# Kernel tuning notes

Hardware: AMD Instinct MI355X
Metric: run time of the kernel (lower is better)

The kernel has to match this reference:

```python
import jax, jax.numpy as jnp
import numpy as np


def setup_inputs() -> dict:
    key = jax.random.key(0)
    k_x, k_B, k_C, k_D, k_step = jax.random.split(key, 5)
    Bsz, L, H = 8, 4096, 512
    P = 256  # effective state dim = dim_ssm_state // 2 (conj_sym)
    # s4d_inv init for Lambda (complex, stored as real/imag parts)
    n = jnp.arange(P, dtype=jnp.float32)
    Lambda_re = -0.5 * jnp.ones((P,), dtype=jnp.float32)
    Lambda_im = (P / np.pi) * (P / (2.0 * n + 1.0) - 1.0)
    # lecun_normal-ish init for B (P,H,2) and C (H,P,2), divided by sqrt(2)
    B = jax.random.normal(k_B, (P, H, 2), dtype=jnp.float32) * (1.0 / np.sqrt(H)) / np.sqrt(2.0)
    C = jax.random.normal(k_C, (H, P, 2), dtype=jnp.float32) * (1.0 / np.sqrt(P)) / np.sqrt(2.0)
    D = jax.random.normal(k_D, (H,), dtype=jnp.float32)
    dt_min, dt_max = 1e-3, 1e-1
    log_step = jax.random.uniform(k_step, (P,)) * (np.log(dt_max) - np.log(dt_min)) + np.log(dt_min)
    x = jax.random.normal(k_x, (Bsz, L, H), dtype=jnp.float32)
    return {"x": x, "Lambda_re": Lambda_re, "Lambda_im": Lambda_im,
            "B": B, "C": C, "D": D, "log_step": log_step.astype(jnp.float32)}


def _binary_op(q_i, q_j):
    A_i, b_i = q_i
    A_j, b_j = q_j
    return (A_j * A_i, A_j * b_i + b_j)


def reference(x, Lambda_re, Lambda_im, B, C, D, log_step):
    # Assemble complex params (conj_sym=True)
    Lam = Lambda_re + 1j * Lambda_im          # (P,)
    B_tilde = B[..., 0] + 1j * B[..., 1]      # (P,H)
    C_tilde = C[..., 0] + 1j * C[..., 1]      # (H,P)
    step = jnp.exp(log_step)                  # (P,) step_rescale = 1.0
    # ZOH discretization
    Lambda_bar = jnp.exp(Lam * step)                              # (P,)
    B_bar = ((Lambda_bar - 1.0) / Lam)[:, None] * B_tilde         # (P,H)
    # Bu elements: (Bsz, L, P) complex
    Bu = jnp.einsum('blh,ph->blp', x.astype(B_bar.dtype), B_bar)
    Lam_elems = jnp.broadcast_to(Lambda_bar, Bu.shape)
    # Parallel linear recurrence over time axis
    _, xs = jax.lax.associative_scan(_binary_op, (Lam_elems, Bu), axis=1)
    # Output projection with conjugate symmetry + D skip
    ys = 2.0 * jnp.einsum('blp,hp->blh', xs, C_tilde).real + D * x
    return ys
```

## Files before the change

kernel.cpp:

```cpp
#include <hip/hip_runtime.h>
#include <hip/hip_bf16.h>
#include <hip/hip_fp16.h>
#include <math.h>

#define BSZ 8
#define LSEQ 4096
#define HDIM 512
#define PDIM 256
#define MROWS (BSZ * LSEQ)
#define NDIM 512
#define CHUNK 32
#define NCHUNK (LSEQ / CHUNK)
#define LOG2CHUNK 5

typedef __attribute__((ext_vector_type(8))) short bf16x8;
typedef __attribute__((ext_vector_type(4))) float f32x4;

__global__ void precompute_params(const float* __restrict__ Lre,
                                  const float* __restrict__ Lim,
                                  const float* __restrict__ logstep,
                                  float* __restrict__ f_re, float* __restrict__ f_im,
                                  float* __restrict__ a_re, float* __restrict__ a_im,
                                  float* __restrict__ al_re, float* __restrict__ al_im) {
    int p = threadIdx.x;
    if (p >= PDIM) return;
    double step = exp((double)logstep[p]);
    double dlr = (double)Lre[p], dli = (double)Lim[p];
    double mag = exp(dlr * step);
    double ar = mag * cos(dli * step);
    double ai = mag * sin(dli * step);
    double den = dlr * dlr + dli * dli;
    double nr = ar - 1.0, ni = ai;
    f_re[p] = (float)((nr * dlr + ni * dli) / den);
    f_im[p] = (float)((ni * dlr - nr * dli) / den);
    a_re[p] = (float)ar;
    a_im[p] = (float)ai;
    double cr = ar, ci = ai;
#pragma unroll
    for (int i = 0; i < LOG2CHUNK; ++i) {
        double tr = cr * cr - ci * ci;
        double ti = 2.0 * cr * ci;
        cr = tr; ci = ti;
    }
    al_re[p] = (float)cr;
    al_im[p] = (float)ci;
}

#define NCONV (MROWS * HDIM / 4 / 256)
__global__ __launch_bounds__(256) void prep(
    const float* __restrict__ x, __hip_bfloat16* __restrict__ xb,
    const float* __restrict__ f_re, const float* __restrict__ f_im,
    const float* __restrict__ Bmat, __hip_bfloat16* __restrict__ W1T,
    const float* __restrict__ Cmat, __hip_bfloat16* __restrict__ W2T) {
    const int bid = blockIdx.x;
    const int tid = threadIdx.x;
    if (bid < NCONV) {
        int i = bid * 256 + tid;
        float4 v = ((const float4*)x)[i];
        union { ushort4 u; __hip_bfloat16 h[4]; } o;
        o.h[0] = __float2bfloat16(v.x);
        o.h[1] = __float2bfloat16(v.y);
        o.h[2] = __float2bfloat16(v.z);
        o.h[3] = __float2bfloat16(v.w);
        ((ushort4*)xb)[i] = o.u;
    } else if (bid < NCONV + 512) {
        int idx = (bid - NCONV) * 256 + tid;
        int p = idx / HDIM, h = idx % HDIM;
        float fr = f_re[p], fi = f_im[p];
        float br = Bmat[(size_t)(p * HDIM + h) * 2 + 0];
        float bi = Bmat[(size_t)(p * HDIM + h) * 2 + 1];
        W1T[(size_t)(2 * p) * HDIM + h]     = __float2bfloat16(fr * br - fi * bi);
        W1T[(size_t)(2 * p + 1) * HDIM + h] = __float2bfloat16(fr * bi + fi * br);
    } else {
        int idx = (bid - NCONV - 512) * 256 + tid;
        int h = idx / PDIM, p = idx % PDIM;
        float cr = Cmat[(size_t)(h * PDIM + p) * 2 + 0];
        float ci = Cmat[(size_t)(h * PDIM + p) * 2 + 1];
        W2T[(size_t)h * NDIM + 2 * p]     = __float2bfloat16(2.0f * cr);
        W2T[(size_t)h * NDIM + 2 * p + 1] = __float2bfloat16(-2.0f * ci);
    }
}

template <typename OT, bool SKIP>
__global__ __launch_bounds__(256) void gemm_bt(
    const __hip_bfloat16* __restrict__ A,
    const __hip_bfloat16* __restrict__ BT,
    OT* __restrict__ C,
    const float* __restrict__ Dvec,
    const __hip_bfloat16* __restrict__ Xskip,
    int M, int N, int K) {
    __shared__ __hip_bfloat16 smA[3 * 128 * 32];
    __shared__ __hip_bfloat16 smB[3 * 128 * 32];

    const int tid = threadIdx.x;
    const int lane = tid & 63;
    const int wave = tid >> 6;
    const int row0 = blockIdx.x * 128;
    const int col0 = blockIdx.y * 128;
    const int wm = (wave >> 1) * 64;
    const int wn = (wave & 1) * 64;

    const int sr = lane >> 2;
    const int swz_st = ((lane >> 2) & 3) ^ ((lane >> 4) & 3);
    const int sk = (((lane & 3) ^ swz_st) * 8);
    const int quad = lane >> 4;
    const int l15 = lane & 15;
    const int rq = ((quad ^ ((l15 & 3) ^ ((l15 >> 2) & 3))) * 8);

    f32x4 acc[4][4] = {};

    auto stage = [&](int buf, int t) {
        const int k0 = t << 5;
#pragma unroll
        for (int q = 0; q < 2; ++q) {
            const int chunk = wave * 32 + q * 16;
            const __hip_bfloat16* gA = A + (size_t)(row0 + chunk + sr) * K + k0 + sk;
            __builtin_amdgcn_global_load_lds(
                (const __attribute__((address_space(1))) void*)gA,
                (__attribute__((address_space(3))) void*)&smA[buf * 4096 + chunk * 32],
                16, 0, 0);
            const __hip_bfloat16* gB = BT + (size_t)(col0 + chunk + sr) * K + k0 + sk;
            __builtin_amdgcn_global_load_lds(
                (const __attribute__((address_space(1))) void*)gB,
                (__attribute__((address_space(3))) void*)&smB[buf * 4096 + chunk * 32],
                16, 0, 0);
        }
    };

    const int nk = K >> 5;
    stage(0, 0);
    stage(1, 1);
    asm volatile("s_waitcnt vmcnt(4)" ::: "memory");
    __builtin_amdgcn_s_barrier();

    int cur = 0;
    for (int t = 0; t < nk; ++t) {
        if (t + 2 < nk) {
            int st = cur + 2; if (st >= 3) st -= 3;
            stage(st, t + 2);
        }

        const __hip_bfloat16* sA = &smA[cur * 4096];
        const __hip_bfloat16* sB = &smB[cur * 4096];
        bf16x8 af[4], bfr[4];
#pragma unroll
        for (int i = 0; i < 4; ++i)
            af[i] = *(const bf16x8*)&sA[(wm + i * 16 + l15) * 32 + rq];
#pragma unroll
        for (int j = 0; j < 4; ++j)
            bfr[j] = *(const bf16x8*)&sB[(wn + j * 16 + l15) * 32 + rq];
#pragma unroll
        for (int i = 0; i < 4; ++i)
#pragma unroll
            for (int j = 0; j < 4; ++j)
                acc[i][j] = __builtin_amdgcn_mfma_f32_16x16x32_bf16(
                    af[i], bfr[j], acc[i][j], 0, 0, 0);

        if (t + 1 < nk) {
            if (t + 2 < nk)
                asm volatile("s_waitcnt vmcnt(4)" ::: "memory");
            else
                asm volatile("s_waitcnt vmcnt(0)" ::: "memory");
            __builtin_amdgcn_s_barrier();
        }
        cur += 1; if (cur == 3) cur = 0;
    }

#pragma unroll
    for (int i = 0; i < 4; ++i) {
        const int mbase = row0 + wm + i * 16 + quad * 4;
#pragma unroll
        for (int j = 0; j < 4; ++j) {
            const int col = col0 + wn + j * 16 + l15;
            const float dv = SKIP ? Dvec[col] : 0.0f;
#pragma unroll
            for (int r = 0; r < 4; ++r) {
                const size_t m = (size_t)(mbase + r);
                float v = acc[i][j][r];
                if (SKIP) v += dv * __bfloat162float(Xskip[m * N + col]);
                if constexpr (sizeof(OT) == 2) {
                    C[m * N + col] = OT(v);
                } else {
                    C[m * N + col] = v;
                }
            }
        }
    }
}

__global__ __launch_bounds__(256) void scan_chunks(const __half2* __restrict__ Bu2,
                                                   const float* __restrict__ a_re,
                                                   const float* __restrict__ a_im,
                                                   float2* __restrict__ S) {
    int b = blockIdx.x / NCHUNK;
    int c = blockIdx.x % NCHUNK;
    int p = threadIdx.x;
    float ar = a_re[p], ai = a_im[p];
    float sr = 0.0f, si = 0.0f;
    size_t m0 = (size_t)b * LSEQ + (size_t)c * CHUNK;
    for (int j = 0; j < CHUNK; ++j) {
        float2 u = __half22float2(Bu2[(m0 + j) * PDIM + p]);
        float nsr = ar * sr - ai * si + u.x;
        float nsi = ar * si + ai * sr + u.y;
        sr = nsr; si = nsi;
    }
    S[(size_t)(b * NCHUNK + c) * PDIM + p] = make_float2(sr, si);
}

__global__ __launch_bounds__(256) void scan_carry(const float2* __restrict__ S,
                                                  const float* __restrict__ al_re,
                                                  const float* __restrict__ al_im,
                                                  float2* __restrict__ carry) {
    const int wid = blockIdx.x * 4 + (threadIdx.x >> 6);
    const int b = wid >> 8;
    const int p = wid & 255;
    const int lane = threadIdx.x & 63;
    const int c0 = 2 * lane, c1 = 2 * lane + 1;
    float alr = al_re[p], ali = al_im[p];
    float2 s0 = S[(size_t)(b * NCHUNK + c0) * PDIM + p];
    float2 s1 = S[(size_t)(b * NCHUNK + c1) * PDIM + p];
    float Ar = alr * alr - ali * ali;
    float Ai = 2.0f * alr * ali;
    float br = alr * s0.x - ali * s0.y + s1.x;
    float bi = alr * s0.y + ali * s0.x + s1.y;
#pragma unroll
    for (int d = 1; d < 64; d <<= 1) {
        float pAr = __shfl_up(Ar, d);
        float pAi = __shfl_up(Ai, d);
        float pbr = __shfl_up(br, d);
        float pbi = __shfl_up(bi, d);
        if (lane >= d) {
            float nAr = Ar * pAr - Ai * pAi;
            float nAi = Ar * pAi + Ai * pAr;
            float nbr = Ar * pbr - Ai * pbi + br;
            float nbi = Ar * pbi + Ai * pbr + bi;
            Ar = nAr; Ai = nAi; br = nbr; bi = nbi;
        }
    }
    float er = __shfl_up(br, 1);
    float ei = __shfl_up(bi, 1);
    if (lane == 0) { er = 0.0f; ei = 0.0f; }
    carry[(size_t)(b * NCHUNK + c0) * PDIM + p] = make_float2(er, ei);
    carry[(size_t)(b * NCHUNK + c1) * PDIM + p] =
        make_float2(alr * er - ali * ei + s0.x, alr * ei + ali * er + s0.y);
}

__global__ __launch_bounds__(256) void scan_apply(const __half2* __restrict__ Bu2,
                                                  const float* __restrict__ a_re,
                                                  const float* __restrict__ a_im,
                                                  const float2* __restrict__ carry,
                                                  ushort2* __restrict__ xsb2) {
    int b = blockIdx.x / NCHUNK;
    int c = blockIdx.x % NCHUNK;
    int p = threadIdx.x;
    float ar = a_re[p], ai = a_im[p];
    float2 c0 = carry[(size_t)(b * NCHUNK + c) * PDIM + p];
    float sr = c0.x, si = c0.y;
    size_t m0 = (size_t)b * LSEQ + (size_t)c * CHUNK;
    for (int j = 0; j < CHUNK; ++j) {
        size_t idx = (m0 + j) * PDIM + p;
        float2 u = __half22float2(Bu2[idx]);
        float nsr = ar * sr - ai * si + u.x;
        float nsi = ar * si + ai * sr + u.y;
        sr = nsr; si = nsi;
        union { ushort2 u2; __hip_bfloat16 h[2]; } o;
        o.h[0] = __float2bfloat16(sr);
        o.h[1] = __float2bfloat16(si);
        xsb2[idx] = o.u2;
    }
}

extern "C" void kernel_launch(void* const* d_in, const int* in_sizes, int n_in,
                              void* d_out, int out_size, void* d_ws, size_t ws_size,
                              hipStream_t stream) {
    const float* x       = (const float*)d_in[0];
    const float* Lre     = (const float*)d_in[1];
    const float* Lim     = (const float*)d_in[2];
    const float* Bmat    = (const float*)d_in[3];
    const float* Cmat    = (const float*)d_in[4];
    const float* Dvec    = (const float*)d_in[5];
    const float* logstep = (const float*)d_in[6];
    float* out = (float*)d_out;

    char* ws = (char*)d_ws;
    const size_t MB = 1u << 20;
    __hip_bfloat16* xb  = (__hip_bfloat16*)(ws + 0);
    __hip_bfloat16* xsb = (__hip_bfloat16*)(ws + 32 * MB);
    __half* Bu          = (__half*)(ws + 64 * MB);
    __hip_bfloat16* W1T = (__hip_bfloat16*)(ws + 96 * MB);
    __hip_bfloat16* W2T = (__hip_bfloat16*)(ws + 96 * MB + 512 * 1024);
    float*  a_re  = (float*)(ws + 97 * MB);
    float*  a_im  = (float*)(ws + 97 * MB + 4096);
    float*  f_re  = (float*)(ws + 97 * MB + 8192);
    float*  f_im  = (float*)(ws + 97 * MB + 12288);
    float*  al_re = (float*)(ws + 97 * MB + 16384);
    float*  al_im = (float*)(ws + 97 * MB + 20480);
    float2* S     = (float2*)(ws + 98 * MB);
    float2* carry = (float2*)(ws + 100 * MB);

    precompute_params<<<1, 256, 0, stream>>>(Lre, Lim, logstep,
                                             f_re, f_im, a_re, a_im, al_re, al_im);
    prep<<<NCONV + 1024, 256, 0, stream>>>(x, xb, f_re, f_im, Bmat, W1T, Cmat, W2T);

    dim3 ggrid(MROWS / 128, NDIM / 128);
    gemm_bt<__half, false><<<ggrid, 256, 0, stream>>>(
        xb, W1T, Bu, nullptr, nullptr, MROWS, NDIM, HDIM);

    scan_chunks<<<BSZ * NCHUNK, 256, 0, stream>>>((const __half2*)Bu, a_re, a_im, S);
    scan_carry<<<BSZ * PDIM / 4, 256, 0, stream>>>(S, al_re, al_im, carry);
    scan_apply<<<BSZ * NCHUNK, 256, 0, stream>>>((const __half2*)Bu, a_re, a_im,
                                                 carry, (ushort2*)xsb);

    dim3 ggrid2(MROWS / 128, HDIM / 128);
    gemm_bt<float, true><<<ggrid2, 256, 0, stream>>>(
        xsb, W2T, out, Dvec, xb, MROWS, HDIM, NDIM);
}
```

Measured before the change: 217.6 us.

## Stream A from global with LDS-resident weight slice in both GEMMs

Both GEMMs now use a kernel that loads a full 64-column x 512-K slice of the weight matrix into LDS once per block. Each wave then streams its own 64-row A tiles directly from global into registers with a 3-deep software prefetch, so there is no per-K-step barrier or A staging through LDS. The grid is 512 blocks of 8 groups, each covering 512 rows with a launch-bound occupancy of 2. The trade-off is that A tiles are no longer shared across waves: each wave issues uncoalesced 16-byte row loads, and every column group re-reads the whole A matrix.

```diff
diff --git a/kernel.cpp b/kernel.cpp
--- a/kernel.cpp
+++ b/kernel.cpp
@@ -81,107 +81,91 @@
     }
 }
 
+#define WROWB 1040
+
 template <typename OT, bool SKIP>
-__global__ __launch_bounds__(256) void gemm_bt(
+__global__ __launch_bounds__(256, 2) void gemm_stream(
     const __hip_bfloat16* __restrict__ A,
     const __hip_bfloat16* __restrict__ BT,
     OT* __restrict__ C,
     const float* __restrict__ Dvec,
     const __hip_bfloat16* __restrict__ Xskip,
     int M, int N, int K) {
-    __shared__ __hip_bfloat16 smA[3 * 128 * 32];
-    __shared__ __hip_bfloat16 smB[3 * 128 * 32];
+    __shared__ char smW[64 * WROWB];
 
     const int tid = threadIdx.x;
     const int lane = tid & 63;
     const int wave = tid >> 6;
-    const int row0 = blockIdx.x * 128;
-    const int col0 = blockIdx.y * 128;
-    const int wm = (wave >> 1) * 64;
-    const int wn = (wave & 1) * 64;
-
-    const int sr = lane >> 2;
-    const int swz_st = ((lane >> 2) & 3) ^ ((lane >> 4) & 3);
-    const int sk = (((lane & 3) ^ swz_st) * 8);
+    const int g = blockIdx.x >> 6;
+    const int s = blockIdx.x & 63;
+    const int col0 = g * 64;
     const int quad = lane >> 4;
     const int l15 = lane & 15;
-    const int rq = ((quad ^ ((l15 & 3) ^ ((l15 >> 2) & 3))) * 8);
-
-    f32x4 acc[4][4] = {};
-
-    auto stage = [&](int buf, int t) {
-        const int k0 = t << 5;
-#pragma unroll
-        for (int q = 0; q < 2; ++q) {
-            const int chunk = wave * 32 + q * 16;
-            const __hip_bfloat16* gA = A + (size_t)(row0 + chunk + sr) * K + k0 + sk;
-            __builtin_amdgcn_global_load_lds(
-                (const __attribute__((address_space(1))) void*)gA,
-                (__attribute__((address_space(3))) void*)&smA[buf * 4096 + chunk * 32],
-                16, 0, 0);
-            const __hip_bfloat16* gB = BT + (size_t)(col0 + chunk + sr) * K + k0 + sk;
-            __builtin_amdgcn_global_load_lds(
-                (const __attribute__((address_space(1))) void*)gB,
-                (__attribute__((address_space(3))) void*)&smB[buf * 4096 + chunk * 32],
-                16, 0, 0);
+
+    for (int rr = 0; rr < 16; ++rr) {
+        const int r = wave * 16 + rr;
+        const __hip_bfloat16* gW = BT + (size_t)(col0 + r) * K + lane * 8;
+        __builtin_amdgcn_global_load_lds(
+            (const __attribute__((address_space(1))) void*)gW,
+            (__attribute__((address_space(3))) void*)(smW + r * WROWB),
+            16, 0, 0);
+    }
+    __syncthreads();
+
+    auto ldw = [&](int j, int kf) -> bf16x8 {
+        return *(const bf16x8*)(smW + (j * 16 + l15) * WROWB + kf * 64 + quad * 16);
+    };
+
+    const int nkf = K >> 5;
+#pragma unroll 1
+    for (int cc = 0; cc < 2; ++cc) {
+        const int mrow0 = (s * 8 + wave + cc * 4) * 64;
+
+        f32x4 acc[4][4] = {};
+        bf16x8 a[3][4];
+        auto lda = [&](int kf, int buf) {
+#pragma unroll
+            for (int i = 0; i < 4; ++i) {
+                const __hip_bfloat16* gA =
+                    A + (size_t)(mrow0 + i * 16 + l15) * K + kf * 32 + quad * 8;
+                a[buf][i] = *(const bf16x8*)gA;
+            }
+        };
+
+        lda(0, 0);
+        lda(1, 1);
+#pragma unroll
+        for (int kf = 0; kf < 16; ++kf) {
+            const int buf = kf % 3;
+            if (kf + 2 < 16) lda(kf + 2, (kf + 2) % 3);
+            bf16x8 w0 = ldw(0, kf), w1 = ldw(1, kf),
+                   w2 = ldw(2, kf), w3 = ldw(3, kf);
+#pragma unroll
+            for (int i = 0; i < 4; ++i) {
+                acc[i][0] = __builtin_amdgcn_mfma_f32_16x16x32_bf16(a[buf][i], w0, acc[i][0], 0, 0, 0);
+                acc[i][1] = __builtin_amdgcn_mfma_f32_16x16x32_bf16(a[buf][i], w1, acc[i][1], 0, 0, 0);
+                acc[i][2] = __builtin_amdgcn_mfma_f32_16x16x32_bf16(a[buf][i], w2, acc[i][2], 0, 0, 0);
+                acc[i][3] = __builtin_amdgcn_mfma_f32_16x16x32_bf16(a[buf][i], w3, acc[i][3], 0, 0, 0);
+            }
         }
-    };
-
-    const int nk = K >> 5;
-    stage(0, 0);
-    stage(1, 1);
-    asm volatile("s_waitcnt vmcnt(4)" ::: "memory");
-    __builtin_amdgcn_s_barrier();
-
-    int cur = 0;
-    for (int t = 0; t < nk; ++t) {
-        if (t + 2 < nk) {
-            int st = cur + 2; if (st >= 3) st -= 3;
-            stage(st, t + 2);
-        }
-
-        const __hip_bfloat16* sA = &smA[cur * 4096];
-        const __hip_bfloat16* sB = &smB[cur * 4096];
-        bf16x8 af[4], bfr[4];
-#pragma unroll
-        for (int i = 0; i < 4; ++i)
-            af[i] = *(const bf16x8*)&sA[(wm + i * 16 + l15) * 32 + rq];
-#pragma unroll
-        for (int j = 0; j < 4; ++j)
-            bfr[j] = *(const bf16x8*)&sB[(wn + j * 16 + l15) * 32 + rq];
-#pragma unroll
-        for (int i = 0; i < 4; ++i)
-#pragma unroll
-            for (int j = 0; j < 4; ++j)
-                acc[i][j] = __builtin_amdgcn_mfma_f32_16x16x32_bf16(
-                    af[i], bfr[j], acc[i][j], 0, 0, 0);
-
-        if (t + 1 < nk) {
-            if (t + 2 < nk)
-                asm volatile("s_waitcnt vmcnt(4)" ::: "memory");
-            else
-                asm volatile("s_waitcnt vmcnt(0)" ::: "memory");
-            __builtin_amdgcn_s_barrier();
-        }
-        cur += 1; if (cur == 3) cur = 0;
-    }
-
-#pragma unroll
-    for (int i = 0; i < 4; ++i) {
-        const int mbase = row0 + wm + i * 16 + quad * 4;
-#pragma unroll
-        for (int j = 0; j < 4; ++j) {
-            const int col = col0 + wn + j * 16 + l15;
-            const float dv = SKIP ? Dvec[col] : 0.0f;
-#pragma unroll
-            for (int r = 0; r < 4; ++r) {
-                const size_t m = (size_t)(mbase + r);
-                float v = acc[i][j][r];
-                if (SKIP) v += dv * __bfloat162float(Xskip[m * N + col]);
-                if constexpr (sizeof(OT) == 2) {
-                    C[m * N + col] = OT(v);
-                } else {
-                    C[m * N + col] = v;
+
+#pragma unroll
+        for (int i = 0; i < 4; ++i) {
+            const int mbase = mrow0 + i * 16 + quad * 4;
+#pragma unroll
+            for (int j = 0; j < 4; ++j) {
+                const int col = col0 + j * 16 + l15;
+                const float dv = SKIP ? Dvec[col] : 0.0f;
+#pragma unroll
+                for (int r = 0; r < 4; ++r) {
+                    const size_t m = (size_t)(mbase + r);
+                    float v = acc[i][j][r];
+                    if (SKIP) v += dv * __bfloat162float(Xskip[m * N + col]);
+                    if constexpr (sizeof(OT) == 2) {
+                        C[m * N + col] = OT(v);
+                    } else {
+                        C[m * N + col] = v;
+                    }
                 }
             }
         }
@@ -302,8 +286,7 @@
                                              f_re, f_im, a_re, a_im, al_re, al_im);
     prep<<<NCONV + 1024, 256, 0, stream>>>(x, xb, f_re, f_im, Bmat, W1T, Cmat, W2T);
 
-    dim3 ggrid(MROWS / 128, NDIM / 128);
-    gemm_bt<__half, false><<<ggrid, 256, 0, stream>>>(
+    gemm_stream<__half, false><<<512, 256, 0, stream>>>(
         xb, W1T, Bu, nullptr, nullptr, MROWS, NDIM, HDIM);
 
     scan_chunks<<<BSZ * NCHUNK, 256, 0, stream>>>((const __half2*)Bu, a_re, a_im, S);
@@ -311,7 +294,6 @@
     scan_apply<<<BSZ * NCHUNK, 256, 0, stream>>>((const __half2*)Bu, a_re, a_im,
                                                  carry, (ushort2*)xsb);
 
-    dim3 ggrid2(MROWS / 128, HDIM / 128);
-    gemm_bt<float, true><<<ggrid2, 256, 0, stream>>>(
+    gemm_stream<float, true><<<512, 256, 0, stream>>>(
         xsb, W2T, out, Dvec, xb, MROWS, HDIM, NDIM);
 }
```

Result: slower. 314.7 us (+44.6%).

## Fold carry scan into apply kernel and vectorize scan to two states per thread

Applied to the files above, without the earlier changes.

Removes the separate scan_carry kernel. Each scan_apply thread now serially combines the preceding chunk summaries to get its own carry. Both scan kernels also handle two state channels per thread with 8-byte loads and stores, and pack two chunks per block, giving 512 blocks. This saves one launch and the carry buffer round-trip, but adds a serial loop of up to 127 steps over S per thread, so later chunks do more redundant work.

```diff
diff --git a/kernel.cpp b/kernel.cpp
--- a/kernel.cpp
+++ b/kernel.cpp
@@ -188,85 +188,87 @@
     }
 }
 
-__global__ __launch_bounds__(256) void scan_chunks(const __half2* __restrict__ Bu2,
-                                                   const float* __restrict__ a_re,
-                                                   const float* __restrict__ a_im,
-                                                   float2* __restrict__ S) {
-    int b = blockIdx.x / NCHUNK;
-    int c = blockIdx.x % NCHUNK;
-    int p = threadIdx.x;
-    float ar = a_re[p], ai = a_im[p];
-    float sr = 0.0f, si = 0.0f;
-    size_t m0 = (size_t)b * LSEQ + (size_t)c * CHUNK;
+__global__ __launch_bounds__(256) void scan_chunks(
+    const uint2* __restrict__ Bu4,
+    const float* __restrict__ a_re, const float* __restrict__ a_im,
+    float2* __restrict__ S) {
+    const int bid = blockIdx.x;
+    const int tid = threadIdx.x;
+    const int b = bid >> 6;
+    const int chunk = ((bid & 63) << 1) | (tid >> 7);
+    const int t = tid & 127;
+    const int p0 = t * 2;
+    const size_t m0 = (size_t)b * LSEQ + (size_t)chunk * CHUNK;
+
+    const float a0r = a_re[p0],     a0i = a_im[p0];
+    const float a1r = a_re[p0 + 1], a1i = a_im[p0 + 1];
+
+    float s0r = 0, s0i = 0, s1r = 0, s1i = 0;
+#pragma unroll
     for (int j = 0; j < CHUNK; ++j) {
-        float2 u = __half22float2(Bu2[(m0 + j) * PDIM + p]);
-        float nsr = ar * sr - ai * si + u.x;
-        float nsi = ar * si + ai * sr + u.y;
-        sr = nsr; si = nsi;
-    }
-    S[(size_t)(b * NCHUNK + c) * PDIM + p] = make_float2(sr, si);
-}
-
-__global__ __launch_bounds__(256) void scan_carry(const float2* __restrict__ S,
-                                                  const float* __restrict__ al_re,
-                                                  const float* __restrict__ al_im,
-                                                  float2* __restrict__ carry) {
-    const int wid = blockIdx.x * 4 + (threadIdx.x >> 6);
-    const int b = wid >> 8;
-    const int p = wid & 255;
-    const int lane = threadIdx.x & 63;
-    const int c0 = 2 * lane, c1 = 2 * lane + 1;
-    float alr = al_re[p], ali = al_im[p];
-    float2 s0 = S[(size_t)(b * NCHUNK + c0) * PDIM + p];
-    float2 s1 = S[(size_t)(b * NCHUNK + c1) * PDIM + p];
-    float Ar = alr * alr - ali * ali;
-    float Ai = 2.0f * alr * ali;
-    float br = alr * s0.x - ali * s0.y + s1.x;
-    float bi = alr * s0.y + ali * s0.x + s1.y;
-#pragma unroll
-    for (int d = 1; d < 64; d <<= 1) {
-        float pAr = __shfl_up(Ar, d);
-        float pAi = __shfl_up(Ai, d);
-        float pbr = __shfl_up(br, d);
-        float pbi = __shfl_up(bi, d);
-        if (lane >= d) {
-            float nAr = Ar * pAr - Ai * pAi;
-            float nAi = Ar * pAi + Ai * pAr;
-            float nbr = Ar * pbr - Ai * pbi + br;
-            float nbi = Ar * pbi + Ai * pbr + bi;
-            Ar = nAr; Ai = nAi; br = nbr; bi = nbi;
-        }
-    }
-    float er = __shfl_up(br, 1);
-    float ei = __shfl_up(bi, 1);
-    if (lane == 0) { er = 0.0f; ei = 0.0f; }
-    carry[(size_t)(b * NCHUNK + c0) * PDIM + p] = make_float2(er, ei);
-    carry[(size_t)(b * NCHUNK + c1) * PDIM + p] =
-        make_float2(alr * er - ali * ei + s0.x, alr * ei + ali * er + s0.y);
-}
-
-__global__ __launch_bounds__(256) void scan_apply(const __half2* __restrict__ Bu2,
-                                                  const float* __restrict__ a_re,
-                                                  const float* __restrict__ a_im,
-                                                  const float2* __restrict__ carry,
-                                                  ushort2* __restrict__ xsb2) {
-    int b = blockIdx.x / NCHUNK;
-    int c = blockIdx.x % NCHUNK;
-    int p = threadIdx.x;
-    float ar = a_re[p], ai = a_im[p];
-    float2 c0 = carry[(size_t)(b * NCHUNK + c) * PDIM + p];
-    float sr = c0.x, si = c0.y;
-    size_t m0 = (size_t)b * LSEQ + (size_t)c * CHUNK;
+        uint2 v = Bu4[(m0 + j) * 128 + t];
+        union { unsigned w; __half2 h; } c0, c1;
+        c0.w = v.x; c1.w = v.y;
+        float2 u0 = __half22float2(c0.h);
+        float2 u1 = __half22float2(c1.h);
+        float n0r = a0r * s0r - a0i * s0i + u0.x;
+        float n0i = a0r * s0i + a0i * s0r + u0.y;
+        float n1r = a1r * s1r - a1i * s1i + u1.x;
+        float n1i = a1r * s1i + a1i * s1r + u1.y;
+        s0r = n0r; s0i = n0i; s1r = n1r; s1i = n1i;
+    }
+    ((float4*)S)[(size_t)(b * NCHUNK + chunk) * 128 + t] =
+        make_float4(s0r, s0i, s1r, s1i);
+}
+
+__global__ __launch_bounds__(256) void scan_apply(
+    const uint2* __restrict__ Bu4,
+    const float* __restrict__ a_re, const float* __restrict__ a_im,
+    const float* __restrict__ al_re, const float* __restrict__ al_im,
+    const float2* __restrict__ S,
+    ushort4* __restrict__ xsb4) {
+    const int bid = blockIdx.x;
+    const int tid = threadIdx.x;
+    const int b = bid >> 6;
+    const int chunk = ((bid & 63) << 1) | (tid >> 7);
+    const int t = tid & 127;
+    const int p0 = t * 2;
+    const size_t m0 = (size_t)b * LSEQ + (size_t)chunk * CHUNK;
+
+    const float a0r = a_re[p0],      a0i = a_im[p0];
+    const float a1r = a_re[p0 + 1],  a1i = a_im[p0 + 1];
+    const float l0r = al_re[p0],     l0i = al_im[p0];
+    const float l1r = al_re[p0 + 1], l1i = al_im[p0 + 1];
+
+    const float4* S4 = (const float4*)S;
+    float s0r = 0, s0i = 0, s1r = 0, s1i = 0;
+    for (int c = 0; c < chunk; ++c) {
+        float4 s = S4[(size_t)(b * NCHUNK + c) * 128 + t];
+        float n0r = l0r * s0r - l0i * s0i + s.x;
+        float n0i = l0r * s0i + l0i * s0r + s.y;
+        float n1r = l1r * s1r - l1i * s1i + s.z;
+        float n1i = l1r * s1i + l1i * s1r + s.w;
+        s0r = n0r; s0i = n0i; s1r = n1r; s1i = n1i;
+    }
+
+#pragma unroll
     for (int j = 0; j < CHUNK; ++j) {
-        size_t idx = (m0 + j) * PDIM + p;
-        float2 u = __half22float2(Bu2[idx]);
-        float nsr = ar * sr - ai * si + u.x;
-        float nsi = ar * si + ai * sr + u.y;
-        sr = nsr; si = nsi;
-        union { ushort2 u2; __hip_bfloat16 h[2]; } o;
-        o.h[0] = __float2bfloat16(sr);
-        o.h[1] = __float2bfloat16(si);
-        xsb2[idx] = o.u2;
+        uint2 v = Bu4[(m0 + j) * 128 + t];
+        union { unsigned w; __half2 h; } c0, c1;
+        c0.w = v.x; c1.w = v.y;
+        float2 u0 = __half22float2(c0.h);
+        float2 u1 = __half22float2(c1.h);
+        float n0r = a0r * s0r - a0i * s0i + u0.x;
+        float n0i = a0r * s0i + a0i * s0r + u0.y;
+        float n1r = a1r * s1r - a1i * s1i + u1.x;
+        float n1i = a1r * s1i + a1i * s1r + u1.y;
+        s0r = n0r; s0i = n0i; s1r = n1r; s1i = n1i;
+        union { ushort4 w4; __hip_bfloat16 h[4]; } o;
+        o.h[0] = __float2bfloat16(s0r);
+        o.h[1] = __float2bfloat16(s0i);
+        o.h[2] = __float2bfloat16(s1r);
+        o.h[3] = __float2bfloat16(s1i);
+        xsb4[(m0 + j) * 128 + t] = o.w4;
     }
 }
 
@@ -296,7 +298,6 @@
     float*  al_re = (float*)(ws + 97 * MB + 16384);
     float*  al_im = (float*)(ws + 97 * MB + 20480);
     float2* S     = (float2*)(ws + 98 * MB);
-    float2* carry = (float2*)(ws + 100 * MB);
 
     precompute_params<<<1, 256, 0, stream>>>(Lre, Lim, logstep,
                                              f_re, f_im, a_re, a_im, al_re, al_im);
@@ -306,10 +307,9 @@
     gemm_bt<__half, false><<<ggrid, 256, 0, stream>>>(
         xb, W1T, Bu, nullptr, nullptr, MROWS, NDIM, HDIM);
 
-    scan_chunks<<<BSZ * NCHUNK, 256, 0, stream>>>((const __half2*)Bu, a_re, a_im, S);
-    scan_carry<<<BSZ * PDIM / 4, 256, 0, stream>>>(S, al_re, al_im, carry);
-    scan_apply<<<BSZ * NCHUNK, 256, 0, stream>>>((const __half2*)Bu, a_re, a_im,
-                                                 carry, (ushort2*)xsb);
+    scan_chunks<<<512, 256, 0, stream>>>((const uint2*)Bu, a_re, a_im, S);
+    scan_apply<<<512, 256, 0, stream>>>((const uint2*)Bu, a_re, a_im,
+                                        al_re, al_im, S, (ushort4*)xsb);
 
     dim3 ggrid2(MROWS / 128, HDIM / 128);
     gemm_bt<float, true><<<ggrid2, 256, 0, stream>>>(
```

Result: slower. 242.2 us (+11.3%).

## Fuse fp32-to-bf16 conversion of x into first GEMM's A-tile loading

Applied to the files above, without the earlier changes.

Drops the separate pass that converted x to bf16. The first GEMM now reads fp32 x directly through registers, converts it, and writes bf16 into LDS with double buffering, while B still streams through global_load_lds. The skip term in the second GEMM now reads fp32 x directly. This removes a 64MB read and 32MB write of conversion traffic, at the cost of twice the A-operand global reads in GEMM1 and fp32 reads in the epilogue. GEMM1 also moves to a simpler 2-stage pipeline with full __syncthreads.

```diff
diff --git a/kernel.cpp b/kernel.cpp
--- a/kernel.cpp
+++ b/kernel.cpp
@@ -46,25 +46,14 @@
     al_im[p] = (float)ci;
 }
 
-#define NCONV (MROWS * HDIM / 4 / 256)
-__global__ __launch_bounds__(256) void prep(
-    const float* __restrict__ x, __hip_bfloat16* __restrict__ xb,
+__global__ __launch_bounds__(256) void prep_w(
     const float* __restrict__ f_re, const float* __restrict__ f_im,
     const float* __restrict__ Bmat, __hip_bfloat16* __restrict__ W1T,
     const float* __restrict__ Cmat, __hip_bfloat16* __restrict__ W2T) {
     const int bid = blockIdx.x;
     const int tid = threadIdx.x;
-    if (bid < NCONV) {
-        int i = bid * 256 + tid;
-        float4 v = ((const float4*)x)[i];
-        union { ushort4 u; __hip_bfloat16 h[4]; } o;
-        o.h[0] = __float2bfloat16(v.x);
-        o.h[1] = __float2bfloat16(v.y);
-        o.h[2] = __float2bfloat16(v.z);
-        o.h[3] = __float2bfloat16(v.w);
-        ((ushort4*)xb)[i] = o.u;
-    } else if (bid < NCONV + 512) {
-        int idx = (bid - NCONV) * 256 + tid;
+    if (bid < 512) {
+        int idx = bid * 256 + tid;
         int p = idx / HDIM, h = idx % HDIM;
         float fr = f_re[p], fi = f_im[p];
         float br = Bmat[(size_t)(p * HDIM + h) * 2 + 0];
@@ -72,7 +61,7 @@
         W1T[(size_t)(2 * p) * HDIM + h]     = __float2bfloat16(fr * br - fi * bi);
         W1T[(size_t)(2 * p + 1) * HDIM + h] = __float2bfloat16(fr * bi + fi * br);
     } else {
-        int idx = (bid - NCONV - 512) * 256 + tid;
+        int idx = (bid - 512) * 256 + tid;
         int h = idx / PDIM, p = idx % PDIM;
         float cr = Cmat[(size_t)(h * PDIM + p) * 2 + 0];
         float ci = Cmat[(size_t)(h * PDIM + p) * 2 + 1];
@@ -81,13 +70,124 @@
     }
 }
 
-template <typename OT, bool SKIP>
-__global__ __launch_bounds__(256) void gemm_bt(
+__global__ __launch_bounds__(256) void gemm_xw(
+    const float* __restrict__ A,
+    const __hip_bfloat16* __restrict__ BT,
+    __half* __restrict__ C,
+    int M, int N, int K) {
+    __shared__ __hip_bfloat16 smA[2 * 128 * 32];
+    __shared__ __hip_bfloat16 smB[2 * 128 * 32];
+
+    const int tid = threadIdx.x;
+    const int lane = tid & 63;
+    const int wave = tid >> 6;
+    const int row0 = blockIdx.x * 128;
+    const int col0 = blockIdx.y * 128;
+    const int wm = (wave >> 1) * 64;
+    const int wn = (wave & 1) * 64;
+
+    const int sr = lane >> 2;
+    const int swz_st = ((lane >> 2) & 3) ^ ((lane >> 4) & 3);
+    const int sk = (((lane & 3) ^ swz_st) * 8);
+    const int quad = lane >> 4;
+    const int l15 = lane & 15;
+    const int rq = ((quad ^ ((l15 & 3) ^ ((l15 >> 2) & 3))) * 8);
+
+    f32x4 acc[4][4] = {};
+
+    auto stageB = [&](int buf, int t) {
+        const int k0 = t << 5;
+#pragma unroll
+        for (int q = 0; q < 2; ++q) {
+            const int chunk = wave * 32 + q * 16;
+            const __hip_bfloat16* gB = BT + (size_t)(col0 + chunk + sr) * K + k0 + sk;
+            __builtin_amdgcn_global_load_lds(
+                (const __attribute__((address_space(1))) void*)gB,
+                (__attribute__((address_space(3))) void*)&smB[buf * 4096 + chunk * 32],
+                16, 0, 0);
+        }
+    };
+    auto loadA = [&](int t, float4* ar) {
+        const int k0 = t << 5;
+#pragma unroll
+        for (int q = 0; q < 2; ++q) {
+            const float* gA = A + (size_t)(row0 + wave * 32 + q * 16 + sr) * K + k0 + sk;
+            ar[q * 2]     = *(const float4*)gA;
+            ar[q * 2 + 1] = *(const float4*)(gA + 4);
+        }
+    };
+    auto writeA = [&](int buf, const float4* ar) {
+#pragma unroll
+        for (int q = 0; q < 2; ++q) {
+            union { bf16x8 v; __hip_bfloat16 h[8]; } o;
+            o.h[0] = __float2bfloat16(ar[q * 2].x);
+            o.h[1] = __float2bfloat16(ar[q * 2].y);
+            o.h[2] = __float2bfloat16(ar[q * 2].z);
+            o.h[3] = __float2bfloat16(ar[q * 2].w);
+            o.h[4] = __float2bfloat16(ar[q * 2 + 1].x);
+            o.h[5] = __float2bfloat16(ar[q * 2 + 1].y);
+            o.h[6] = __float2bfloat16(ar[q * 2 + 1].z);
+            o.h[7] = __float2bfloat16(ar[q * 2 + 1].w);
+            *(bf16x8*)&smA[buf * 4096 + (wave * 32 + q * 16 + sr) * 32 + (lane & 3) * 8] = o.v;
+        }
+    };
+
+    const int nk = K >> 5;
+    float4 ar[4];
+    loadA(0, ar);
+    stageB(0, 0);
+    writeA(0, ar);
+    __syncthreads();
+
+    int buf = 0;
+    for (int t = 0; t < nk; ++t) {
+        if (t + 1 < nk) {
+            loadA(t + 1, ar);
+            stageB(buf ^ 1, t + 1);
+        }
+
+        const __hip_bfloat16* sA = &smA[buf * 4096];
+        const __hip_bfloat16* sB = &smB[buf * 4096];
+        bf16x8 af[4], bfr[4];
+#pragma unroll
+        for (int i = 0; i < 4; ++i)
+            af[i] = *(const bf16x8*)&sA[(wm + i * 16 + l15) * 32 + rq];
+#pragma unroll
+        for (int j = 0; j < 4; ++j)
+            bfr[j] = *(const bf16x8*)&sB[(wn + j * 16 + l15) * 32 + rq];
+#pragma unroll
+        for (int i = 0; i < 4; ++i)
+#pragma unroll
+            for (int j = 0; j < 4; ++j)
+                acc[i][j] = __builtin_amdgcn_mfma_f32_16x16x32_bf16(
+                    af[i], bfr[j], acc[i][j], 0, 0, 0);
+
+        if (t + 1 < nk) writeA(buf ^ 1, ar);
+        __syncthreads();
+        buf ^= 1;
+    }
+
+#pragma unroll
+    for (int i = 0; i < 4; ++i) {
+        const int mbase = row0 + wm + i * 16 + quad * 4;
+#pragma unroll
+        for (int j = 0; j < 4; ++j) {
+            const int col = col0 + wn + j * 16 + l15;
+#pragma unroll
+            for (int r = 0; r < 4; ++r) {
+                const size_t m = (size_t)(mbase + r);
+                C[m * N + col] = __half(acc[i][j][r]);
+            }
+        }
+    }
+}
+
+__global__ __launch_bounds__(256) void gemm_bt_skip(
     const __hip_bfloat16* __restrict__ A,
     const __hip_bfloat16* __restrict__ BT,
-    OT* __restrict__ C,
+    float* __restrict__ C,
     const float* __restrict__ Dvec,
-    const __hip_bfloat16* __restrict__ Xskip,
+    const float* __restrict__ Xskip,
     int M, int N, int K) {
     __shared__ __hip_bfloat16 smA[3 * 128 * 32];
     __shared__ __hip_bfloat16 smB[3 * 128 * 32];
@@ -172,17 +272,11 @@
 #pragma unroll
         for (int j = 0; j < 4; ++j) {
             const int col = col0 + wn + j * 16 + l15;
-            const float dv = SKIP ? Dvec[col] : 0.0f;
+            const float dv = Dvec[col];
 #pragma unroll
             for (int r = 0; r < 4; ++r) {
                 const size_t m = (size_t)(mbase + r);
-                float v = acc[i][j][r];
-                if (SKIP) v += dv * __bfloat162float(Xskip[m * N + col]);
-                if constexpr (sizeof(OT) == 2) {
-                    C[m * N + col] = OT(v);
-                } else {
-                    C[m * N + col] = v;
-                }
+                C[m * N + col] = acc[i][j][r] + dv * Xskip[m * N + col];
             }
         }
     }
@@ -284,27 +378,25 @@
 
     char* ws = (char*)d_ws;
     const size_t MB = 1u << 20;
-    __hip_bfloat16* xb  = (__hip_bfloat16*)(ws + 0);
-    __hip_bfloat16* xsb = (__hip_bfloat16*)(ws + 32 * MB);
-    __half* Bu          = (__half*)(ws + 64 * MB);
-    __hip_bfloat16* W1T = (__hip_bfloat16*)(ws + 96 * MB);
-    __hip_bfloat16* W2T = (__hip_bfloat16*)(ws + 96 * MB + 512 * 1024);
-    float*  a_re  = (float*)(ws + 97 * MB);
-    float*  a_im  = (float*)(ws + 97 * MB + 4096);
-    float*  f_re  = (float*)(ws + 97 * MB + 8192);
-    float*  f_im  = (float*)(ws + 97 * MB + 12288);
-    float*  al_re = (float*)(ws + 97 * MB + 16384);
-    float*  al_im = (float*)(ws + 97 * MB + 20480);
-    float2* S     = (float2*)(ws + 98 * MB);
-    float2* carry = (float2*)(ws + 100 * MB);
+    __hip_bfloat16* xsb = (__hip_bfloat16*)(ws + 0);
+    __half* Bu          = (__half*)(ws + 32 * MB);
+    __hip_bfloat16* W1T = (__hip_bfloat16*)(ws + 64 * MB);
+    __hip_bfloat16* W2T = (__hip_bfloat16*)(ws + 64 * MB + 512 * 1024);
+    float*  a_re  = (float*)(ws + 65 * MB);
+    float*  a_im  = (float*)(ws + 65 * MB + 4096);
+    float*  f_re  = (float*)(ws + 65 * MB + 8192);
+    float*  f_im  = (float*)(ws + 65 * MB + 12288);
+    float*  al_re = (float*)(ws + 65 * MB + 16384);
+    float*  al_im = (float*)(ws + 65 * MB + 20480);
+    float2* S     = (float2*)(ws + 66 * MB);
+    float2* carry = (float2*)(ws + 68 * MB);
 
     precompute_params<<<1, 256, 0, stream>>>(Lre, Lim, logstep,
                                              f_re, f_im, a_re, a_im, al_re, al_im);
-    prep<<<NCONV + 1024, 256, 0, stream>>>(x, xb, f_re, f_im, Bmat, W1T, Cmat, W2T);
+    prep_w<<<1024, 256, 0, stream>>>(f_re, f_im, Bmat, W1T, Cmat, W2T);
 
     dim3 ggrid(MROWS / 128, NDIM / 128);
-    gemm_bt<__half, false><<<ggrid, 256, 0, stream>>>(
-        xb, W1T, Bu, nullptr, nullptr, MROWS, NDIM, HDIM);
+    gemm_xw<<<ggrid, 256, 0, stream>>>(x, W1T, Bu, MROWS, NDIM, HDIM);
 
     scan_chunks<<<BSZ * NCHUNK, 256, 0, stream>>>((const __half2*)Bu, a_re, a_im, S);
     scan_carry<<<BSZ * PDIM / 4, 256, 0, stream>>>(S, al_re, al_im, carry);
@@ -312,6 +404,6 @@
                                                  carry, (ushort2*)xsb);
 
     dim3 ggrid2(MROWS / 128, HDIM / 128);
-    gemm_bt<float, true><<<ggrid2, 256, 0, stream>>>(
-        xsb, W2T, out, Dvec, xb, MROWS, HDIM, NDIM);
-}
+    gemm_bt_skip<<<ggrid2, 256, 0, stream>>>(
+        xsb, W2T, out, Dvec, x, MROWS, HDIM, NDIM);
+}
```

After: 215.7 us. No clear change (-0.9%).
